# Kernel optimization log

Hardware: AMD Instinct MI355X
Metric: run time of the kernel (lower is better)

## Reference

```python
import jax, jax.numpy as jnp
import numpy as np

B, S, D = 4, 2048, 1024
E, K, I = 8, 2, 2752  # num_experts, top_k, intermediate_size (64*ceil(1024*8/3/64))


def setup_inputs() -> dict:
    key = jax.random.key(0)
    k0, k1, k2, k3, k4 = jax.random.split(key, 5)
    return {
        "x": jax.random.normal(k0, (B, S, D), jnp.float32),
        "router_w": jax.random.normal(k1, (D, E), jnp.float32) * 0.02,   # gate Linear, no bias
        "w_gate": jax.random.normal(k2, (E, D, I), jnp.float32) * 0.02,  # per-expert gate proj
        "w_up": jax.random.normal(k3, (E, D, I), jnp.float32) * 0.02,    # per-expert up proj
        "w_down": jax.random.normal(k4, (E, I, D), jnp.float32) * 0.02,  # per-expert down proj
    }


def reference(x, router_w, w_gate, w_up, w_down):
    orig_shape = x.shape
    d = orig_shape[-1]
    xf = x.reshape(-1, d)                      # [T, D]
    T = xf.shape[0]
    n_experts = router_w.shape[1]

    # Router: softmax over all experts, then top-k and renormalize (matches torch order).
    probs = jax.nn.softmax(xf @ router_w, axis=-1)        # [T, E]
    w, idx = jax.lax.top_k(probs, K)                       # [T, K]
    w = w / (jnp.sum(w, axis=-1, keepdims=True) + 1e-6)

    # Dense combine weights: combine[t, e] = routing weight of expert e for token t (0 if unrouted).
    combine = jnp.zeros((T, n_experts), xf.dtype).at[jnp.arange(T)[:, None], idx].add(w)

    # Per-expert GatedMLP (SwiGLU, no bias, dropout=0 in eval): Down(SiLU(Gate(x)) * Up(x)).
    out = jnp.zeros_like(xf)
    for e in range(n_experts):  # fixed small expert count; data dims stay vectorized
        h = jax.nn.silu(xf @ w_gate[e]) * (xf @ w_up[e])   # [T, I]
        out = out + combine[:, e:e + 1] * (h @ w_down[e])  # scatter-combine
    return out.reshape(orig_shape)
```

## Files before the change

kernel.cpp:

```cpp
#include <hip/hip_runtime.h>
#include <hip/hip_bf16.h>
#include <math.h>

#define T_TOKENS 8192
#define D_MODEL  1024
#define N_EXP    8
#define I_RAW    2752
#define I_PAD    2816
#define N_CAT    5632
#define MAXROWS  18432
#define NYT      72
#define DUMP_SID (2 * T_TOKENS)

typedef __attribute__((ext_vector_type(8))) short bf16x8;
typedef __attribute__((ext_vector_type(8))) unsigned short ushort8;
typedef __attribute__((ext_vector_type(4))) float f32x4;
typedef unsigned short ushort_t;

#define CTRL_COUNT 0
#define CTRL_CUR   8
#define CTRL_SEG   16
#define CTRL_YT    32

#define VMW(n)  asm volatile("s_waitcnt vmcnt(" n ")" ::: "memory")
#define BARRIER() asm volatile("s_barrier" ::: "memory")

__device__ __forceinline__ void gll16(const void* g, void* l) {
  __builtin_amdgcn_global_load_lds(
      (const __attribute__((address_space(1))) void*)g,
      (__attribute__((address_space(3))) void*)l, 16, 0, 0);
}

__device__ __forceinline__ float silu_mul(float g, float u) {
  return g / (1.f + __expf(-g)) * u;
}

__device__ __forceinline__ float bf2f(ushort_t u) {
  return __uint_as_float((unsigned)u << 16);
}

__global__ void __launch_bounds__(64) router_kernel(
    const float* __restrict__ x, const float* __restrict__ rw,
    int* __restrict__ topidx, float* __restrict__ topw) {
  const int t = blockIdx.x;
  const int lane = threadIdx.x;
  const float* xr = x + (size_t)t * D_MODEL;
  float acc[N_EXP];
#pragma unroll
  for (int e = 0; e < N_EXP; ++e) acc[e] = 0.f;
  for (int d = lane; d < D_MODEL; d += 64) {
    const float xv = xr[d];
    const float* r = rw + (size_t)d * N_EXP;
#pragma unroll
    for (int e = 0; e < N_EXP; ++e) acc[e] = fmaf(xv, r[e], acc[e]);
  }
#pragma unroll
  for (int e = 0; e < N_EXP; ++e) {
    for (int off = 32; off > 0; off >>= 1) acc[e] += __shfl_xor(acc[e], off, 64);
  }
  if (lane == 0) {
    float m = acc[0];
#pragma unroll
    for (int e = 1; e < N_EXP; ++e) m = fmaxf(m, acc[e]);
    float p[N_EXP], s = 0.f;
#pragma unroll
    for (int e = 0; e < N_EXP; ++e) { p[e] = expf(acc[e] - m); s += p[e]; }
    int i0 = 0; float v0 = p[0];
#pragma unroll
    for (int e = 1; e < N_EXP; ++e) if (p[e] > v0) { v0 = p[e]; i0 = e; }
    int i1 = -1; float v1 = -1.f;
#pragma unroll
    for (int e = 0; e < N_EXP; ++e) if (e != i0 && p[e] > v1) { v1 = p[e]; i1 = e; }
    v0 /= s; v1 /= s;
    const float r = v0 + v1 + 1e-6f;
    v0 /= r; v1 /= r;
    topidx[t * 2] = i0; topidx[t * 2 + 1] = i1;
    topw[t * 2] = v0;  topw[t * 2 + 1] = v1;
  }
}

__global__ void __launch_bounds__(512) hist_kernel(
    const int* __restrict__ topidx, int* __restrict__ ctrl) {
  __shared__ int lh[N_EXP];
  const int tid = threadIdx.x;
  if (tid < N_EXP) lh[tid] = 0;
  __syncthreads();
  const int g = blockIdx.x * 512 + tid;
  atomicAdd(&lh[topidx[g]], 1);
  __syncthreads();
  if (tid < N_EXP) atomicAdd(&ctrl[CTRL_COUNT + tid], lh[tid]);
}

__global__ void cvt_x_kernel(const float* __restrict__ x,
                             __hip_bfloat16* __restrict__ xb, int n4) {
  const int i = blockIdx.x * blockDim.x + threadIdx.x;
  if (i < n4) {
    const float4 v = ((const float4*)x)[i];
    __hip_bfloat16 b0 = __float2bfloat16(v.x), b1 = __float2bfloat16(v.y);
    __hip_bfloat16 b2 = __float2bfloat16(v.z), b3 = __float2bfloat16(v.w);
    ushort4 o;
    o.x = reinterpret_cast<ushort_t&>(b0); o.y = reinterpret_cast<ushort_t&>(b1);
    o.z = reinterpret_cast<ushort_t&>(b2); o.w = reinterpret_cast<ushort_t&>(b3);
    ((ushort4*)xb)[i] = o;
  }
}

__global__ void __launch_bounds__(256) transpose_cvt_kernel(
    const float* __restrict__ in, __hip_bfloat16* __restrict__ out,
    int Rin, int Cin, int Co, long in_es, long out_es, int mode) {
  __shared__ float tile[64][65];
  const float* inp = in + (size_t)blockIdx.z * in_es;
  __hip_bfloat16* outp = out + (size_t)blockIdx.z * out_es;
  const int b0 = blockIdx.x * 64;
  const int a0 = blockIdx.y * 64;
  const int tid = threadIdx.x;
  const bool inb = (b0 < Rin) && (a0 < Cin);
  const int bi0 = tid >> 4, a4 = (tid & 15) * 4;
  if (inb) {
#pragma unroll
    for (int i = 0; i < 4; ++i) {
      const int bi = bi0 + i * 16;
      const float4 v = *(const float4*)&inp[(size_t)(b0 + bi) * Cin + a0 + a4];
      tile[bi][a4] = v.x; tile[bi][a4 + 1] = v.y;
      tile[bi][a4 + 2] = v.z; tile[bi][a4 + 3] = v.w;
    }
  } else {
#pragma unroll
    for (int i = 0; i < 4; ++i) {
      const int bi = bi0 + i * 16;
      tile[bi][a4] = 0.f; tile[bi][a4 + 1] = 0.f;
      tile[bi][a4 + 2] = 0.f; tile[bi][a4 + 3] = 0.f;
    }
  }
  __syncthreads();
#pragma unroll
  for (int half = 0; half < 2; ++half) {
    const int g = tid + half * 256;
    const int al = g >> 3, bc = (g & 7) * 8;
    ushort8 o;
#pragma unroll
    for (int j = 0; j < 8; ++j) {
      __hip_bfloat16 h = __float2bfloat16(tile[bc + j][al]);
      o[j] = *(const ushort_t*)&h;
    }
    const int a = a0 + al;
    int A;
    if (mode == 0) A = a;
    else A = ((a >> 5) << 6) + ((mode == 2) ? 32 : 0) + (a & 31);
    *(ushort8*)&outp[(size_t)A * Co + b0 + bc] = o;
  }
}

__global__ void padfill_kernel(int* __restrict__ rowmap, float* __restrict__ roww) {
  const int i = blockIdx.x * blockDim.x + threadIdx.x;
  if (i < MAXROWS) { rowmap[i] = DUMP_SID; roww[i] = 0.f; }
}

__global__ void scan_kernel(int* __restrict__ ctrl) {
  if (threadIdx.x == 0 && blockIdx.x == 0) {
    int s = 0, yt = 0;
    ctrl[CTRL_SEG] = 0;
    for (int e = 0; e < N_EXP; ++e) {
      const int c = ctrl[CTRL_COUNT + e];
      const int padded = (c + 255) & ~255;
      const int n = padded >> 8;
      for (int j = 0; j < n; ++j) ctrl[CTRL_YT + yt + j] = e;
      yt += n;
      s += padded;
      ctrl[CTRL_SEG + 1 + e] = s;
    }
    for (; yt < NYT; ++yt) ctrl[CTRL_YT + yt] = -1;
  }
}

__global__ void __launch_bounds__(512) scatter_kernel(
    const int* __restrict__ topidx, const float* __restrict__ topw,
    int* __restrict__ ctrl, int* __restrict__ rowmap,
    float* __restrict__ roww) {
  __shared__ int lh[N_EXP];
  __shared__ int lbase[N_EXP];
  const int tid = threadIdx.x;
  if (tid < N_EXP) lh[tid] = 0;
  __syncthreads();
  const int g = blockIdx.x * 512 + tid;
  const int e = topidx[g];
  const int rank = atomicAdd(&lh[e], 1);
  __syncthreads();
  if (tid < N_EXP) lbase[tid] = atomicAdd(&ctrl[CTRL_CUR + tid], lh[tid]);
  __syncthreads();
  const int pos = ctrl[CTRL_SEG + e] + lbase[e] + rank;
  rowmap[pos] = g;
  roww[pos] = topw[g];
}

__global__ void __launch_bounds__(512, 2) gemm1_kernel(
    const __hip_bfloat16* __restrict__ xb,
    const __hip_bfloat16* __restrict__ wcat,
    __hip_bfloat16* __restrict__ H,
    const int* __restrict__ rowmap, const float* __restrict__ roww,
    const int* __restrict__ ctrl) {
  const unsigned b = blockIdx.x;
  const int xcd = b & 7;
  const unsigned w = b >> 3;
  const int yt = xcd * 9 + (int)(w % 9);
  const int xn = (int)(w / 9);
  const int e = ctrl[CTRL_YT + yt];
  if (e < 0) return;
  const int row0 = yt * 256;
  const int nbase = xn * 256;
  const int tid = threadIdx.x, lane = tid & 63, wid = tid >> 6;
  const int wrm = (wid >> 2) * 128, wrn = (wid & 3) * 64;

  __shared__ __align__(16) __hip_bfloat16 sA[2][2][8192];
  __shared__ __align__(16) __hip_bfloat16 sB[2][2][8192];
  __shared__ float sW[256];

  if (tid < 256) sW[tid] = roww[row0 + tid];

  const int srow = tid >> 2;
  const int kc = ((tid & 3) - ((tid >> 3) & 3)) & 3;
  int tok0 = rowmap[row0 + srow] >> 1;
  int tok1 = rowmap[row0 + 128 + srow] >> 1;
  tok0 = min(tok0, T_TOKENS - 1);
  tok1 = min(tok1, T_TOKENS - 1);
  const __hip_bfloat16* gA0 = xb + (size_t)tok0 * D_MODEL + kc * 8;
  const __hip_bfloat16* gA1 = xb + (size_t)tok1 * D_MODEL + kc * 8;
  const __hip_bfloat16* gB0 = wcat + ((size_t)e * N_CAT + nbase + srow) * D_MODEL + kc * 8;
  const __hip_bfloat16* gB1 = gB0 + (size_t)128 * D_MODEL;

  __syncthreads();

  auto stageA = [&](int sl_, int kh, int kt) {
    const int ko = kt * 64 + kh * 32;
    gll16(gA0 + ko, &sA[sl_][kh][tid * 8]);
    gll16(gA1 + ko, &sA[sl_][kh][4096 + tid * 8]);
  };
  auto stageB = [&](int sl_, int kh, int kt) {
    const int ko = kt * 64 + kh * 32;
    gll16(gB0 + ko, &sB[sl_][kh][tid * 8]);
    gll16(gB1 + ko, &sB[sl_][kh][4096 + tid * 8]);
  };

  f32x4 acc[8][4];
  const f32x4 z4 = {0.f, 0.f, 0.f, 0.f};
#pragma unroll
  for (int a_ = 0; a_ < 8; ++a_)
#pragma unroll
    for (int b_ = 0; b_ < 4; ++b_) acc[a_][b_] = z4;

  const int poff = ((lane >> 4) + ((lane & 15) >> 1)) & 3;
  const int arow = (wrm + (lane & 15)) * 32 + poff * 8;
  const int brow = (wrn + (lane & 15)) * 32 + poff * 8;

  const int NT = D_MODEL / 64;
  stageA(0, 0, 0); stageB(0, 0, 0);
  stageA(0, 1, 0); stageB(0, 1, 0);
  stageA(1, 0, 1); stageB(1, 0, 1);
  VMW("8"); BARRIER();

#define G1_HALF(SL, KH, T, STG_A, STG_B)                                       \
  {                                                                            \
    bf16x8 aLo[4], aHi[4], bfv[4];                                             \
    _Pragma("unroll")                                                          \
    for (int mi = 0; mi < 4; ++mi)                                             \
      aLo[mi] = *(const bf16x8*)&sA[SL][KH][arow + mi * 512];                  \
    _Pragma("unroll")                                                          \
    for (int ni = 0; ni < 4; ++ni)                                             \
      bfv[ni] = *(const bf16x8*)&sB[SL][KH][brow + ni * 512];                  \
    STG_A;                                                                     \
    BARRIER();                                                                 \
    __builtin_amdgcn_s_setprio(1);                                             \
    _Pragma("unroll")                                                          \
    for (int mi = 0; mi < 4; ++mi)                                             \
      _Pragma("unroll")                                                        \
      for (int ni = 0; ni < 4; ++ni)                                           \
        acc[mi][ni] = __builtin_amdgcn_mfma_f32_16x16x32_bf16(aLo[mi], bfv[ni], acc[mi][ni], 0, 0, 0); \
    __builtin_amdgcn_s_setprio(0);                                             \
    BARRIER();                                                                 \
    _Pragma("unroll")                                                          \
    for (int mi = 0; mi < 4; ++mi)                                             \
      aHi[mi] = *(const bf16x8*)&sA[SL][KH][arow + (4 + mi) * 512];            \
    STG_B;                                                                     \
    VMW("8");                                                                  \
    BARRIER();                                                                 \
    __builtin_amdgcn_s_setprio(1);                                             \
    _Pragma("unroll")                                                          \
    for (int mi = 0; mi < 4; ++mi)                                             \
      _Pragma("unroll")                                                        \
      for (int ni = 0; ni < 4; ++ni)                                           \
        acc[4 + mi][ni] = __builtin_amdgcn_mfma_f32_16x16x32_bf16(aHi[mi], bfv[ni], acc[4 + mi][ni], 0, 0, 0); \
    __builtin_amdgcn_s_setprio(0);                                             \
    BARRIER();                                                                 \
  }

#define G1_KTILE(SL, T)                                                        \
  {                                                                            \
    const int tn1 = ((T) + 1 < NT) ? (T) + 1 : 0;                              \
    const int tn2 = ((T) + 2 < NT) ? (T) + 2 : 0;                              \
    G1_HALF(SL, 0, T, stageA(1 - (SL), 1, tn1), stageB(1 - (SL), 1, tn1))      \
    G1_HALF(SL, 1, T, stageA((SL), 0, tn2),     stageB((SL), 0, tn2))          \
  }

  for (int t = 0; t < NT; t += 2) {
    G1_KTILE(0, t)
    G1_KTILE(1, t + 1)
  }

  const int hcolbase = ((nbase + wrn) >> 6) * 32;
#pragma unroll
  for (int mi = 0; mi < 8; ++mi) {
    const int r0 = wrm + mi * 16 + ((lane >> 4) * 4);
#pragma unroll
    for (int ni = 0; ni < 2; ++ni) {
      const int hcol = hcolbase + ni * 16 + (lane & 15);
      const f32x4 g = acc[mi][ni], u = acc[mi][ni + 2];
#pragma unroll
      for (int j = 0; j < 4; ++j) {
        const float h = silu_mul(g[j], u[j]) * sW[r0 + j];
        H[(size_t)(row0 + r0 + j) * I_PAD + hcol] = __float2bfloat16(h);
      }
    }
  }
}

__global__ void __launch_bounds__(256, 3) gemm2_kernel(
    const __hip_bfloat16* __restrict__ H,
    const __hip_bfloat16* __restrict__ wdt,
    ushort_t* __restrict__ slot,
    const int* __restrict__ rowmap, const int* __restrict__ ctrl) {
  const unsigned b = blockIdx.x;
  const int xcd = b & 7;
  const unsigned w = b >> 3;
  const int mt = xcd * 18 + (int)(w % 18);
  const int xn = (int)(w / 18);
  const int e = ctrl[CTRL_YT + (mt >> 1)];
  if (e < 0) return;
  const int row0 = mt * 128;
  const int nbase = xn * 128;
  const int tid = threadIdx.x, lane = tid & 63, wid = tid >> 6;
  const int wr = (wid >> 1) * 64, wc = (wid & 1) * 64;

  __shared__ __align__(16) __hip_bfloat16 sA[128 * 64];
  __shared__ __align__(16) __hip_bfloat16 sB[128 * 64];
  __shared__ int sTok[128];

  if (tid < 128) sTok[tid] = rowmap[row0 + tid];

  const __hip_bfloat16* gA[4];
  const __hip_bfloat16* gB[4];
#pragma unroll
  for (int i = 0; i < 4; ++i) {
    const int c = i * 256 + tid;
    const int row = c >> 3;
    const int kc8 = ((c & 7) - row) & 7;
    gA[i] = H + (size_t)(row0 + row) * I_PAD + kc8 * 8;
    gB[i] = wdt + ((size_t)e * D_MODEL + nbase + row) * I_PAD + kc8 * 8;
  }

  f32x4 acc[4][4];
  const f32x4 z4 = {0.f, 0.f, 0.f, 0.f};
#pragma unroll
  for (int a_ = 0; a_ < 4; ++a_)
#pragma unroll
    for (int b_ = 0; b_ < 4; ++b_) acc[a_][b_] = z4;

  const int NT = I_PAD / 64;
  for (int kt = 0; kt < NT; ++kt) {
    __syncthreads();
#pragma unroll
    for (int i = 0; i < 4; ++i) {
      const int c = i * 256 + tid;
      gll16(gA[i] + kt * 64, &sA[c * 8]);
      gll16(gB[i] + kt * 64, &sB[c * 8]);
    }
    __syncthreads();
#pragma unroll
    for (int ks = 0; ks < 2; ++ks) {
      bf16x8 a[4], bb[4];
#pragma unroll
      for (int mi = 0; mi < 4; ++mi) {
        const int row = wr + mi * 16 + (lane & 15);
        const int p = (ks * 4 + (lane >> 4) + row) & 7;
        a[mi] = *(const bf16x8*)&sA[row * 64 + p * 8];
      }
#pragma unroll
      for (int ni = 0; ni < 4; ++ni) {
        const int row = wc + ni * 16 + (lane & 15);
        const int p = (ks * 4 + (lane >> 4) + row) & 7;
        bb[ni] = *(const bf16x8*)&sB[row * 64 + p * 8];
      }
      __builtin_amdgcn_s_setprio(1);
#pragma unroll
      for (int mi = 0; mi < 4; ++mi)
#pragma unroll
        for (int ni = 0; ni < 4; ++ni)
          acc[mi][ni] = __builtin_amdgcn_mfma_f32_16x16x32_bf16(a[mi], bb[ni], acc[mi][ni], 0, 0, 0);
      __builtin_amdgcn_s_setprio(0);
    }
  }

#pragma unroll
  for (int mi = 0; mi < 4; ++mi) {
    const int r0 = wr + mi * 16 + ((lane >> 4) * 4);
#pragma unroll
    for (int ni = 0; ni < 4; ++ni) {
      const int col = nbase + wc + ni * 16 + (lane & 15);
#pragma unroll
      for (int j = 0; j < 4; ++j) {
        const int sid = sTok[r0 + j];
        __hip_bfloat16 hv = __float2bfloat16(acc[mi][ni][j]);
        slot[(size_t)sid * D_MODEL + col] = *(const ushort_t*)&hv;
      }
    }
  }
}

__global__ void __launch_bounds__(256) combine_kernel(
    const ushort_t* __restrict__ slot, float* __restrict__ out) {
  const int i = blockIdx.x * 256 + threadIdx.x;
  const int t = i >> 7;
  const int c = (i & 127) << 3;
  const size_t b0 = ((size_t)(t << 1)) * D_MODEL + c;
  const ushort8 a = *(const ushort8*)&slot[b0];
  const ushort8 b = *(const ushort8*)&slot[b0 + D_MODEL];
  float4 o0, o1;
  o0.x = bf2f(a[0]) + bf2f(b[0]); o0.y = bf2f(a[1]) + bf2f(b[1]);
  o0.z = bf2f(a[2]) + bf2f(b[2]); o0.w = bf2f(a[3]) + bf2f(b[3]);
  o1.x = bf2f(a[4]) + bf2f(b[4]); o1.y = bf2f(a[5]) + bf2f(b[5]);
  o1.z = bf2f(a[6]) + bf2f(b[6]); o1.w = bf2f(a[7]) + bf2f(b[7]);
  ((float4*)out)[i * 2] = o0;
  ((float4*)out)[i * 2 + 1] = o1;
}

extern "C" void kernel_launch(void* const* d_in, const int* in_sizes, int n_in,
                              void* d_out, int out_size, void* d_ws, size_t ws_size,
                              hipStream_t stream) {
  (void)in_sizes; (void)n_in; (void)ws_size; (void)out_size;
  const float* x  = (const float*)d_in[0];
  const float* rw = (const float*)d_in[1];
  const float* wg = (const float*)d_in[2];
  const float* wu = (const float*)d_in[3];
  const float* wd = (const float*)d_in[4];
  float* out = (float*)d_out;

  char* ws = (char*)d_ws;
  size_t off = 0;
  auto alloc = [&](size_t bytes) -> char* {
    char* p = ws + off;
    off += (bytes + 255) & ~(size_t)255;
    return p;
  };

  int*   ctrl   = (int*)alloc(512);
  int*   topidx = (int*)alloc((size_t)T_TOKENS * 2 * 4);
  float* topw   = (float*)alloc((size_t)T_TOKENS * 2 * 4);
  int*   rowmap = (int*)alloc((size_t)MAXROWS * 4);
  float* roww   = (float*)alloc((size_t)MAXROWS * 4);
  __hip_bfloat16* xb   = (__hip_bfloat16*)alloc((size_t)T_TOKENS * D_MODEL * 2);
  __hip_bfloat16* wcat = (__hip_bfloat16*)alloc((size_t)N_EXP * N_CAT * D_MODEL * 2);
  __hip_bfloat16* Hbuf = (__hip_bfloat16*)alloc((size_t)MAXROWS * I_PAD * 2);
  ushort_t* slotout = (ushort_t*)alloc((size_t)(2 * T_TOKENS + 1) * D_MODEL * 2);
  __hip_bfloat16* wdt = wcat;

  hipMemsetAsync(ctrl, 0, 256, stream);

  cvt_x_kernel<<<(T_TOKENS * D_MODEL / 4 + 255) / 256, 256, 0, stream>>>(
      x, xb, T_TOKENS * D_MODEL / 4);

  transpose_cvt_kernel<<<dim3(D_MODEL / 64, I_PAD / 64, N_EXP), 256, 0, stream>>>(
      wg, wcat, D_MODEL, I_RAW, D_MODEL, (long)D_MODEL * I_RAW, (long)N_CAT * D_MODEL, 1);
  transpose_cvt_kernel<<<dim3(D_MODEL / 64, I_PAD / 64, N_EXP), 256, 0, stream>>>(
      wu, wcat, D_MODEL, I_RAW, D_MODEL, (long)D_MODEL * I_RAW, (long)N_CAT * D_MODEL, 2);

  router_kernel<<<T_TOKENS, 64, 0, stream>>>(x, rw, topidx, topw);
  hist_kernel<<<(2 * T_TOKENS) / 512, 512, 0, stream>>>(topidx, ctrl);
  padfill_kernel<<<(MAXROWS + 255) / 256, 256, 0, stream>>>(rowmap, roww);
  scan_kernel<<<1, 64, 0, stream>>>(ctrl);
  scatter_kernel<<<(2 * T_TOKENS) / 512, 512, 0, stream>>>(topidx, topw, ctrl, rowmap, roww);

  gemm1_kernel<<<dim3(NYT * 22), 512, 0, stream>>>(
      xb, wcat, Hbuf, rowmap, roww, ctrl);

  transpose_cvt_kernel<<<dim3(I_PAD / 64, D_MODEL / 64, N_EXP), 256, 0, stream>>>(
      wd, wdt, I_RAW, D_MODEL, I_PAD, (long)I_RAW * D_MODEL, (long)D_MODEL * I_PAD, 0);

  gemm2_kernel<<<dim3(NYT * 2 * 8), 256, 0, stream>>>(
      Hbuf, wdt, slotout, rowmap, ctrl);

  combine_kernel<<<(T_TOKENS * D_MODEL / 8) / 256, 256, 0, stream>>>(slotout, out);
}
```

Baseline: 515.7 us.

## Fuse x bf16 conversion into router and shrink gemm1 tiles to 128x128

The bf16 conversion of x now happens inside the router kernel, which already reads x with vectorized float4 loads, so the separate cvt_x pass and one launch go away. gemm1 moves from 256x256 tiles with 512 threads to 128x128 tiles with 256 threads and a 4x larger grid, aiming at better load balance across the padded expert segments and higher occupancy. The cost is less operand reuse per tile and more global traffic. gemm2's launch bounds are raised to 4 blocks per CU, and the ctrl memset is widened to 512 bytes so it covers the per-tile expert table.

```diff
diff --git a/kernel.cpp b/kernel.cpp
--- a/kernel.cpp
+++ b/kernel.cpp
@@ -41,18 +41,31 @@
 
 __global__ void __launch_bounds__(64) router_kernel(
     const float* __restrict__ x, const float* __restrict__ rw,
-    int* __restrict__ topidx, float* __restrict__ topw) {
+    int* __restrict__ topidx, float* __restrict__ topw,
+    __hip_bfloat16* __restrict__ xb) {
   const int t = blockIdx.x;
   const int lane = threadIdx.x;
-  const float* xr = x + (size_t)t * D_MODEL;
+  const float4* xr4 = (const float4*)(x + (size_t)t * D_MODEL);
+  __hip_bfloat16* xbr = xb + (size_t)t * D_MODEL;
   float acc[N_EXP];
 #pragma unroll
   for (int e = 0; e < N_EXP; ++e) acc[e] = 0.f;
-  for (int d = lane; d < D_MODEL; d += 64) {
-    const float xv = xr[d];
-    const float* r = rw + (size_t)d * N_EXP;
-#pragma unroll
-    for (int e = 0; e < N_EXP; ++e) acc[e] = fmaf(xv, r[e], acc[e]);
+#pragma unroll
+  for (int i = 0; i < 4; ++i) {
+    const int f4 = i * 64 + lane;
+    const float4 v = xr4[f4];
+    const int d0 = f4 * 4;
+    const float* r = rw + (size_t)d0 * N_EXP;
+#pragma unroll
+    for (int e = 0; e < N_EXP; ++e)
+      acc[e] = fmaf(v.x, r[e], fmaf(v.y, r[N_EXP + e],
+               fmaf(v.z, r[2 * N_EXP + e], fmaf(v.w, r[3 * N_EXP + e], acc[e]))));
+    __hip_bfloat16 b0 = __float2bfloat16(v.x), b1 = __float2bfloat16(v.y);
+    __hip_bfloat16 b2 = __float2bfloat16(v.z), b3 = __float2bfloat16(v.w);
+    ushort4 o;
+    o.x = *(ushort_t*)&b0; o.y = *(ushort_t*)&b1;
+    o.z = *(ushort_t*)&b2; o.w = *(ushort_t*)&b3;
+    *(ushort4*)&xbr[d0] = o;
   }
 #pragma unroll
   for (int e = 0; e < N_EXP; ++e) {
@@ -89,20 +102,6 @@
   atomicAdd(&lh[topidx[g]], 1);
   __syncthreads();
   if (tid < N_EXP) atomicAdd(&ctrl[CTRL_COUNT + tid], lh[tid]);
-}
-
-__global__ void cvt_x_kernel(const float* __restrict__ x,
-                             __hip_bfloat16* __restrict__ xb, int n4) {
-  const int i = blockIdx.x * blockDim.x + threadIdx.x;
-  if (i < n4) {
-    const float4 v = ((const float4*)x)[i];
-    __hip_bfloat16 b0 = __float2bfloat16(v.x), b1 = __float2bfloat16(v.y);
-    __hip_bfloat16 b2 = __float2bfloat16(v.z), b3 = __float2bfloat16(v.w);
-    ushort4 o;
-    o.x = reinterpret_cast<ushort_t&>(b0); o.y = reinterpret_cast<ushort_t&>(b1);
-    o.z = reinterpret_cast<ushort_t&>(b2); o.w = reinterpret_cast<ushort_t&>(b3);
-    ((ushort4*)xb)[i] = o;
-  }
 }
 
 __global__ void __launch_bounds__(256) transpose_cvt_kernel(
@@ -193,7 +192,7 @@
   roww[pos] = topw[g];
 }
 
-__global__ void __launch_bounds__(512, 2) gemm1_kernel(
+__global__ void __launch_bounds__(256, 2) gemm1_kernel(
     const __hip_bfloat16* __restrict__ xb,
     const __hip_bfloat16* __restrict__ wcat,
     __hip_bfloat16* __restrict__ H,
@@ -202,49 +201,49 @@
   const unsigned b = blockIdx.x;
   const int xcd = b & 7;
   const unsigned w = b >> 3;
-  const int yt = xcd * 9 + (int)(w % 9);
-  const int xn = (int)(w / 9);
-  const int e = ctrl[CTRL_YT + yt];
+  const int mt = xcd * 18 + (int)(w % 18);
+  const int xn = (int)(w / 18);
+  const int e = ctrl[CTRL_YT + (mt >> 1)];
   if (e < 0) return;
-  const int row0 = yt * 256;
-  const int nbase = xn * 256;
+  const int row0 = mt * 128;
+  const int nbase = xn * 128;
   const int tid = threadIdx.x, lane = tid & 63, wid = tid >> 6;
-  const int wrm = (wid >> 2) * 128, wrn = (wid & 3) * 64;
-
-  __shared__ __align__(16) __hip_bfloat16 sA[2][2][8192];
-  __shared__ __align__(16) __hip_bfloat16 sB[2][2][8192];
-  __shared__ float sW[256];
-
-  if (tid < 256) sW[tid] = roww[row0 + tid];
-
-  const int srow = tid >> 2;
+  const int wrm = (wid >> 1) * 64, wrn = (wid & 1) * 64;
+
+  __shared__ __align__(16) __hip_bfloat16 sA[2][2][4096];
+  __shared__ __align__(16) __hip_bfloat16 sB[2][2][4096];
+  __shared__ float sW[128];
+
+  if (tid < 128) sW[tid] = roww[row0 + tid];
+
+  const int r0s = tid >> 2;
   const int kc = ((tid & 3) - ((tid >> 3) & 3)) & 3;
-  int tok0 = rowmap[row0 + srow] >> 1;
-  int tok1 = rowmap[row0 + 128 + srow] >> 1;
-  tok0 = min(tok0, T_TOKENS - 1);
-  tok1 = min(tok1, T_TOKENS - 1);
-  const __hip_bfloat16* gA0 = xb + (size_t)tok0 * D_MODEL + kc * 8;
-  const __hip_bfloat16* gA1 = xb + (size_t)tok1 * D_MODEL + kc * 8;
-  const __hip_bfloat16* gB0 = wcat + ((size_t)e * N_CAT + nbase + srow) * D_MODEL + kc * 8;
-  const __hip_bfloat16* gB1 = gB0 + (size_t)128 * D_MODEL;
+  int tokA0 = rowmap[row0 + r0s] >> 1;
+  int tokA1 = rowmap[row0 + 64 + r0s] >> 1;
+  tokA0 = min(tokA0, T_TOKENS - 1);
+  tokA1 = min(tokA1, T_TOKENS - 1);
+  const __hip_bfloat16* gA0 = xb + (size_t)tokA0 * D_MODEL + kc * 8;
+  const __hip_bfloat16* gA1 = xb + (size_t)tokA1 * D_MODEL + kc * 8;
+  const __hip_bfloat16* gB0 = wcat + ((size_t)e * N_CAT + nbase + r0s) * D_MODEL + kc * 8;
+  const __hip_bfloat16* gB1 = gB0 + (size_t)64 * D_MODEL;
 
   __syncthreads();
 
   auto stageA = [&](int sl_, int kh, int kt) {
     const int ko = kt * 64 + kh * 32;
     gll16(gA0 + ko, &sA[sl_][kh][tid * 8]);
-    gll16(gA1 + ko, &sA[sl_][kh][4096 + tid * 8]);
+    gll16(gA1 + ko, &sA[sl_][kh][2048 + tid * 8]);
   };
   auto stageB = [&](int sl_, int kh, int kt) {
     const int ko = kt * 64 + kh * 32;
     gll16(gB0 + ko, &sB[sl_][kh][tid * 8]);
-    gll16(gB1 + ko, &sB[sl_][kh][4096 + tid * 8]);
+    gll16(gB1 + ko, &sB[sl_][kh][2048 + tid * 8]);
   };
 
-  f32x4 acc[8][4];
+  f32x4 acc[4][4];
   const f32x4 z4 = {0.f, 0.f, 0.f, 0.f};
 #pragma unroll
-  for (int a_ = 0; a_ < 8; ++a_)
+  for (int a_ = 0; a_ < 4; ++a_)
 #pragma unroll
     for (int b_ = 0; b_ < 4; ++b_) acc[a_][b_] = z4;
 
@@ -258,11 +257,11 @@
   stageA(1, 0, 1); stageB(1, 0, 1);
   VMW("8"); BARRIER();
 
-#define G1_HALF(SL, KH, T, STG_A, STG_B)                                       \
+#define G1_HALF(SL, KH, STG_A, STG_B)                                          \
   {                                                                            \
-    bf16x8 aLo[4], aHi[4], bfv[4];                                             \
+    bf16x8 aLo[2], aHi[2], bfv[4];                                             \
     _Pragma("unroll")                                                          \
-    for (int mi = 0; mi < 4; ++mi)                                             \
+    for (int mi = 0; mi < 2; ++mi)                                             \
       aLo[mi] = *(const bf16x8*)&sA[SL][KH][arow + mi * 512];                  \
     _Pragma("unroll")                                                          \
     for (int ni = 0; ni < 4; ++ni)                                             \
@@ -271,24 +270,24 @@
     BARRIER();                                                                 \
     __builtin_amdgcn_s_setprio(1);                                             \
     _Pragma("unroll")                                                          \
-    for (int mi = 0; mi < 4; ++mi)                                             \
+    for (int mi = 0; mi < 2; ++mi)                                             \
       _Pragma("unroll")                                                        \
       for (int ni = 0; ni < 4; ++ni)                                           \
         acc[mi][ni] = __builtin_amdgcn_mfma_f32_16x16x32_bf16(aLo[mi], bfv[ni], acc[mi][ni], 0, 0, 0); \
     __builtin_amdgcn_s_setprio(0);                                             \
     BARRIER();                                                                 \
     _Pragma("unroll")                                                          \
-    for (int mi = 0; mi < 4; ++mi)                                             \
-      aHi[mi] = *(const bf16x8*)&sA[SL][KH][arow + (4 + mi) * 512];            \
+    for (int mi = 0; mi < 2; ++mi)                                             \
+      aHi[mi] = *(const bf16x8*)&sA[SL][KH][arow + (2 + mi) * 512];            \
     STG_B;                                                                     \
     VMW("8");                                                                  \
     BARRIER();                                                                 \
     __builtin_amdgcn_s_setprio(1);                                             \
     _Pragma("unroll")                                                          \
-    for (int mi = 0; mi < 4; ++mi)                                             \
+    for (int mi = 0; mi < 2; ++mi)                                             \
       _Pragma("unroll")                                                        \
       for (int ni = 0; ni < 4; ++ni)                                           \
-        acc[4 + mi][ni] = __builtin_amdgcn_mfma_f32_16x16x32_bf16(aHi[mi], bfv[ni], acc[4 + mi][ni], 0, 0, 0); \
+        acc[2 + mi][ni] = __builtin_amdgcn_mfma_f32_16x16x32_bf16(aHi[mi], bfv[ni], acc[2 + mi][ni], 0, 0, 0); \
     __builtin_amdgcn_s_setprio(0);                                             \
     BARRIER();                                                                 \
   }
@@ -297,8 +296,8 @@
   {                                                                            \
     const int tn1 = ((T) + 1 < NT) ? (T) + 1 : 0;                              \
     const int tn2 = ((T) + 2 < NT) ? (T) + 2 : 0;                              \
-    G1_HALF(SL, 0, T, stageA(1 - (SL), 1, tn1), stageB(1 - (SL), 1, tn1))      \
-    G1_HALF(SL, 1, T, stageA((SL), 0, tn2),     stageB((SL), 0, tn2))          \
+    G1_HALF(SL, 0, stageA(1 - (SL), 1, tn1), stageB(1 - (SL), 1, tn1))         \
+    G1_HALF(SL, 1, stageA((SL), 0, tn2),     stageB((SL), 0, tn2))             \
   }
 
   for (int t = 0; t < NT; t += 2) {
@@ -308,7 +307,7 @@
 
   const int hcolbase = ((nbase + wrn) >> 6) * 32;
 #pragma unroll
-  for (int mi = 0; mi < 8; ++mi) {
+  for (int mi = 0; mi < 4; ++mi) {
     const int r0 = wrm + mi * 16 + ((lane >> 4) * 4);
 #pragma unroll
     for (int ni = 0; ni < 2; ++ni) {
@@ -323,7 +322,7 @@
   }
 }
 
-__global__ void __launch_bounds__(256, 3) gemm2_kernel(
+__global__ void __launch_bounds__(256, 4) gemm2_kernel(
     const __hip_bfloat16* __restrict__ H,
     const __hip_bfloat16* __restrict__ wdt,
     ushort_t* __restrict__ slot,
@@ -462,23 +461,20 @@
   ushort_t* slotout = (ushort_t*)alloc((size_t)(2 * T_TOKENS + 1) * D_MODEL * 2);
   __hip_bfloat16* wdt = wcat;
 
-  hipMemsetAsync(ctrl, 0, 256, stream);
-
-  cvt_x_kernel<<<(T_TOKENS * D_MODEL / 4 + 255) / 256, 256, 0, stream>>>(
-      x, xb, T_TOKENS * D_MODEL / 4);
+  hipMemsetAsync(ctrl, 0, 512, stream);
 
   transpose_cvt_kernel<<<dim3(D_MODEL / 64, I_PAD / 64, N_EXP), 256, 0, stream>>>(
       wg, wcat, D_MODEL, I_RAW, D_MODEL, (long)D_MODEL * I_RAW, (long)N_CAT * D_MODEL, 1);
   transpose_cvt_kernel<<<dim3(D_MODEL / 64, I_PAD / 64, N_EXP), 256, 0, stream>>>(
       wu, wcat, D_MODEL, I_RAW, D_MODEL, (long)D_MODEL * I_RAW, (long)N_CAT * D_MODEL, 2);
 
-  router_kernel<<<T_TOKENS, 64, 0, stream>>>(x, rw, topidx, topw);
+  router_kernel<<<T_TOKENS, 64, 0, stream>>>(x, rw, topidx, topw, xb);
   hist_kernel<<<(2 * T_TOKENS) / 512, 512, 0, stream>>>(topidx, ctrl);
   padfill_kernel<<<(MAXROWS + 255) / 256, 256, 0, stream>>>(rowmap, roww);
   scan_kernel<<<1, 64, 0, stream>>>(ctrl);
   scatter_kernel<<<(2 * T_TOKENS) / 512, 512, 0, stream>>>(topidx, topw, ctrl, rowmap, roww);
 
-  gemm1_kernel<<<dim3(NYT * 22), 512, 0, stream>>>(
+  gemm1_kernel<<<dim3(144 * 44), 256, 0, stream>>>(
       xb, wcat, Hbuf, rowmap, roww, ctrl);
 
   transpose_cvt_kernel<<<dim3(I_PAD / 64, D_MODEL / 64, N_EXP), 256, 0, stream>>>(
```

After: 582.0 us. 1.13x slower.

## Fuse x bf16 conversion into router and simplify gemm1 pipeline barriers

Applied to the files above, without the earlier changes.

The fp32-to-bf16 conversion of x moves into the router kernel, which now reads x with float4 loads, removing a separate kernel and a second read of x. The gemm1 main loop merges its two half-steps into one phase per K-half with a single wait and barrier, loading all 8 A fragments at once. gemm2's launch bound rises to 4 blocks per SM, and the control memset is widened to cover the whole control area. The gemm1 restructure holds more registers live and lengthens the wait before compute, so load overlap may get worse.

```diff
diff --git a/kernel.cpp b/kernel.cpp
--- a/kernel.cpp
+++ b/kernel.cpp
@@ -41,18 +41,31 @@
 
 __global__ void __launch_bounds__(64) router_kernel(
     const float* __restrict__ x, const float* __restrict__ rw,
-    int* __restrict__ topidx, float* __restrict__ topw) {
+    int* __restrict__ topidx, float* __restrict__ topw,
+    __hip_bfloat16* __restrict__ xb) {
   const int t = blockIdx.x;
   const int lane = threadIdx.x;
-  const float* xr = x + (size_t)t * D_MODEL;
+  const float4* xr4 = (const float4*)(x + (size_t)t * D_MODEL);
+  __hip_bfloat16* xbr = xb + (size_t)t * D_MODEL;
   float acc[N_EXP];
 #pragma unroll
   for (int e = 0; e < N_EXP; ++e) acc[e] = 0.f;
-  for (int d = lane; d < D_MODEL; d += 64) {
-    const float xv = xr[d];
-    const float* r = rw + (size_t)d * N_EXP;
-#pragma unroll
-    for (int e = 0; e < N_EXP; ++e) acc[e] = fmaf(xv, r[e], acc[e]);
+#pragma unroll
+  for (int i = 0; i < 4; ++i) {
+    const int f4 = i * 64 + lane;
+    const float4 v = xr4[f4];
+    const int d0 = f4 * 4;
+    const float* r = rw + (size_t)d0 * N_EXP;
+#pragma unroll
+    for (int e = 0; e < N_EXP; ++e)
+      acc[e] = fmaf(v.x, r[e], fmaf(v.y, r[N_EXP + e],
+               fmaf(v.z, r[2 * N_EXP + e], fmaf(v.w, r[3 * N_EXP + e], acc[e]))));
+    __hip_bfloat16 b0 = __float2bfloat16(v.x), b1 = __float2bfloat16(v.y);
+    __hip_bfloat16 b2 = __float2bfloat16(v.z), b3 = __float2bfloat16(v.w);
+    ushort4 o;
+    o.x = *(ushort_t*)&b0; o.y = *(ushort_t*)&b1;
+    o.z = *(ushort_t*)&b2; o.w = *(ushort_t*)&b3;
+    *(ushort4*)&xbr[d0] = o;
   }
 #pragma unroll
   for (int e = 0; e < N_EXP; ++e) {
@@ -89,20 +102,6 @@
   atomicAdd(&lh[topidx[g]], 1);
   __syncthreads();
   if (tid < N_EXP) atomicAdd(&ctrl[CTRL_COUNT + tid], lh[tid]);
-}
-
-__global__ void cvt_x_kernel(const float* __restrict__ x,
-                             __hip_bfloat16* __restrict__ xb, int n4) {
-  const int i = blockIdx.x * blockDim.x + threadIdx.x;
-  if (i < n4) {
-    const float4 v = ((const float4*)x)[i];
-    __hip_bfloat16 b0 = __float2bfloat16(v.x), b1 = __float2bfloat16(v.y);
-    __hip_bfloat16 b2 = __float2bfloat16(v.z), b3 = __float2bfloat16(v.w);
-    ushort4 o;
-    o.x = reinterpret_cast<ushort_t&>(b0); o.y = reinterpret_cast<ushort_t&>(b1);
-    o.z = reinterpret_cast<ushort_t&>(b2); o.w = reinterpret_cast<ushort_t&>(b3);
-    ((ushort4*)xb)[i] = o;
-  }
 }
 
 __global__ void __launch_bounds__(256) transpose_cvt_kernel(
@@ -256,39 +255,25 @@
   stageA(0, 0, 0); stageB(0, 0, 0);
   stageA(0, 1, 0); stageB(0, 1, 0);
   stageA(1, 0, 1); stageB(1, 0, 1);
-  VMW("8"); BARRIER();
-
-#define G1_HALF(SL, KH, T, STG_A, STG_B)                                       \
+
+#define G1_PHASE(SL, KH, STG)                                                  \
   {                                                                            \
-    bf16x8 aLo[4], aHi[4], bfv[4];                                             \
+    VMW("8");                                                                  \
+    BARRIER();                                                                 \
+    bf16x8 af[8], bfv[4];                                                      \
     _Pragma("unroll")                                                          \
-    for (int mi = 0; mi < 4; ++mi)                                             \
-      aLo[mi] = *(const bf16x8*)&sA[SL][KH][arow + mi * 512];                  \
+    for (int mi = 0; mi < 8; ++mi)                                             \
+      af[mi] = *(const bf16x8*)&sA[SL][KH][arow + mi * 512];                   \
     _Pragma("unroll")                                                          \
     for (int ni = 0; ni < 4; ++ni)                                             \
       bfv[ni] = *(const bf16x8*)&sB[SL][KH][brow + ni * 512];                  \
-    STG_A;                                                                     \
-    BARRIER();                                                                 \
+    STG;                                                                       \
     __builtin_amdgcn_s_setprio(1);                                             \
     _Pragma("unroll")                                                          \
-    for (int mi = 0; mi < 4; ++mi)                                             \
+    for (int mi = 0; mi < 8; ++mi)                                             \
       _Pragma("unroll")                                                        \
       for (int ni = 0; ni < 4; ++ni)                                           \
-        acc[mi][ni] = __builtin_amdgcn_mfma_f32_16x16x32_bf16(aLo[mi], bfv[ni], acc[mi][ni], 0, 0, 0); \
-    __builtin_amdgcn_s_setprio(0);                                             \
-    BARRIER();                                                                 \
-    _Pragma("unroll")                                                          \
-    for (int mi = 0; mi < 4; ++mi)                                             \
-      aHi[mi] = *(const bf16x8*)&sA[SL][KH][arow + (4 + mi) * 512];            \
-    STG_B;                                                                     \
-    VMW("8");                                                                  \
-    BARRIER();                                                                 \
-    __builtin_amdgcn_s_setprio(1);                                             \
-    _Pragma("unroll")                                                          \
-    for (int mi = 0; mi < 4; ++mi)                                             \
-      _Pragma("unroll")                                                        \
-      for (int ni = 0; ni < 4; ++ni)                                           \
-        acc[4 + mi][ni] = __builtin_amdgcn_mfma_f32_16x16x32_bf16(aHi[mi], bfv[ni], acc[4 + mi][ni], 0, 0, 0); \
+        acc[mi][ni] = __builtin_amdgcn_mfma_f32_16x16x32_bf16(af[mi], bfv[ni], acc[mi][ni], 0, 0, 0); \
     __builtin_amdgcn_s_setprio(0);                                             \
     BARRIER();                                                                 \
   }
@@ -297,14 +282,15 @@
   {                                                                            \
     const int tn1 = ((T) + 1 < NT) ? (T) + 1 : 0;                              \
     const int tn2 = ((T) + 2 < NT) ? (T) + 2 : 0;                              \
-    G1_HALF(SL, 0, T, stageA(1 - (SL), 1, tn1), stageB(1 - (SL), 1, tn1))      \
-    G1_HALF(SL, 1, T, stageA((SL), 0, tn2),     stageB((SL), 0, tn2))          \
+    G1_PHASE(SL, 0, stageA(1 - (SL), 1, tn1); stageB(1 - (SL), 1, tn1))        \
+    G1_PHASE(SL, 1, stageA((SL), 0, tn2);     stageB((SL), 0, tn2))            \
   }
 
   for (int t = 0; t < NT; t += 2) {
     G1_KTILE(0, t)
     G1_KTILE(1, t + 1)
   }
+  VMW("0");
 
   const int hcolbase = ((nbase + wrn) >> 6) * 32;
 #pragma unroll
@@ -323,7 +309,7 @@
   }
 }
 
-__global__ void __launch_bounds__(256, 3) gemm2_kernel(
+__global__ void __launch_bounds__(256, 4) gemm2_kernel(
     const __hip_bfloat16* __restrict__ H,
     const __hip_bfloat16* __restrict__ wdt,
     ushort_t* __restrict__ slot,
@@ -462,17 +448,14 @@
   ushort_t* slotout = (ushort_t*)alloc((size_t)(2 * T_TOKENS + 1) * D_MODEL * 2);
   __hip_bfloat16* wdt = wcat;
 
-  hipMemsetAsync(ctrl, 0, 256, stream);
-
-  cvt_x_kernel<<<(T_TOKENS * D_MODEL / 4 + 255) / 256, 256, 0, stream>>>(
-      x, xb, T_TOKENS * D_MODEL / 4);
+  hipMemsetAsync(ctrl, 0, 512, stream);
 
   transpose_cvt_kernel<<<dim3(D_MODEL / 64, I_PAD / 64, N_EXP), 256, 0, stream>>>(
       wg, wcat, D_MODEL, I_RAW, D_MODEL, (long)D_MODEL * I_RAW, (long)N_CAT * D_MODEL, 1);
   transpose_cvt_kernel<<<dim3(D_MODEL / 64, I_PAD / 64, N_EXP), 256, 0, stream>>>(
       wu, wcat, D_MODEL, I_RAW, D_MODEL, (long)D_MODEL * I_RAW, (long)N_CAT * D_MODEL, 2);
 
-  router_kernel<<<T_TOKENS, 64, 0, stream>>>(x, rw, topidx, topw);
+  router_kernel<<<T_TOKENS, 64, 0, stream>>>(x, rw, topidx, topw, xb);
   hist_kernel<<<(2 * T_TOKENS) / 512, 512, 0, stream>>>(topidx, ctrl);
   padfill_kernel<<<(MAXROWS + 255) / 256, 256, 0, stream>>>(rowmap, roww);
   scan_kernel<<<1, 64, 0, stream>>>(ctrl);
```

After: 520.5 us. About the same (+0.9%).
